# Kernel tuning notes

Measured on AMD Instinct MI355X. Metric: run time of the kernel, lower is better.

The kernel has to match this reference:

```python
import jax, jax.numpy as jnp
import numpy as np

H, HK, D, BLK, GH = 32, 8, 96, 64, 128   # q heads, kv heads, head_dim, gate block, gate hidden
HIDDEN = 3072
THR = 0.03
NEG = -1e30

def _rot_half(x):
    h = x.shape[-1] // 2
    return jnp.concatenate([-x[..., h:], x[..., :h]], axis=-1)

def setup_inputs() -> dict:
    key = jax.random.key(0)
    ks = jax.random.split(key, 6)
    B, S = 1, 2048
    hidden_states = jax.random.normal(ks[0], (B, S, HIDDEN), dtype=jnp.float32)
    # RoPE tables, theta = 10000
    inv_freq = 1.0 / (10000.0 ** (np.arange(0, D, 2, dtype=np.float32) / D))
    t = np.arange(S, dtype=np.float32)
    freqs = np.outer(t, inv_freq)                   # [S, D/2]
    emb = np.concatenate([freqs, freqs], axis=-1)   # [S, D]
    cos = jnp.asarray(np.cos(emb), dtype=jnp.float32)
    sin = jnp.asarray(np.sin(emb), dtype=jnp.float32)
    op = H * D + 2 * HK * D
    qkv_w = jax.random.normal(ks[1], (HIDDEN, op), dtype=jnp.float32) * 0.02
    o_w = jax.random.normal(ks[2], (H * D, HIDDEN), dtype=jnp.float32) * 0.02
    gate_wq = jax.random.normal(ks[3], (D, GH), dtype=jnp.float32) * 0.05
    gate_wk = jax.random.normal(ks[4], (2 * D, GH), dtype=jnp.float32) * 0.05
    return dict(hidden_states=hidden_states, cos=cos, sin=sin,
                qkv_w=qkv_w, o_w=o_w, gate_wq=gate_wq, gate_wk=gate_wk)

def reference(hidden_states, cos, sin, qkv_w, o_w, gate_wq, gate_wk):
    B, S, _ = hidden_states.shape
    G = H // HK            # GQA group size
    nB = S // BLK          # number of gate blocks
    scale = D ** -0.5

    # fused QKV projection and head split
    qkv = hidden_states @ qkv_w
    q = qkv[..., : H * D].reshape(B, S, H, D)
    k = qkv[..., H * D : H * D + HK * D].reshape(B, S, HK, D)
    v = qkv[..., H * D + HK * D :].reshape(B, S, HK, D)
    q_nope, k_nope = q, k

    # RoPE (unsqueeze over head dim)
    cs = cos[None, :, None, :]
    sn = sin[None, :, None, :]
    q = q * cs + _rot_half(q) * sn
    k = k * cs + _rot_half(k) * sn

    # ---- learned block-sparse gate (SeerAttention AttnGate) ----
    kb = k_nope.reshape(B, nB, BLK, HK, D)
    k_pool = jnp.concatenate([kb.mean(2), kb.max(2)], axis=-1)      # [B,nB,HK,2D] avg+max seq pooling
    k_gate = jnp.einsum('bnhe,eg->bnhg', k_pool, gate_wk)
    q_pool = q_nope.reshape(B, S, HK, G, D).mean(3)                 # q-head pooling to kv heads
    q_pool = q_pool.reshape(B, nB, BLK, HK, D).mean(2)              # block pooling
    q_gate = jnp.einsum('bnhd,dg->bnhg', q_pool, gate_wq)
    gate_logits = jnp.einsum('bqhg,bkhg->bhqk', q_gate, k_gate) * (GH ** -0.5)
    blk_causal = jnp.tril(jnp.ones((nB, nB), dtype=bool))
    gate_logits = jnp.where(blk_causal, gate_logits, NEG)
    gate_probs = jax.nn.softmax(gate_logits, axis=-1)
    block_mask = (gate_probs >= THR) & blk_causal                   # threshold sparsity method
    block_mask = block_mask | jnp.eye(nB, dtype=bool)               # diagonal block always active

    # expand block mask to token level, intersect with causal mask
    tok_mask = jnp.repeat(jnp.repeat(block_mask, BLK, axis=2), BLK, axis=3)  # [B,HK,S,S]
    causal = jnp.tril(jnp.ones((S, S), dtype=bool))
    mask = tok_mask & causal

    # ---- block-sparse masked attention with GQA ----
    qh = q.transpose(0, 2, 1, 3).reshape(B, HK, G, S, D)
    kh = k.transpose(0, 2, 1, 3)                                    # [B,HK,S,D]
    vh = v.transpose(0, 2, 1, 3)
    scores = jnp.einsum('bhgsd,bhtd->bhgst', qh, kh) * scale
    scores = jnp.where(mask[:, :, None], scores, NEG)
    attn = jax.nn.softmax(scores, axis=-1)
    out = jnp.einsum('bhgst,bhtd->bhgsd', attn, vh)                 # [B,HK,G,S,D]
    out = out.reshape(B, H, S, D).transpose(0, 2, 1, 3).reshape(B, S, H * D)
    return out @ o_w
```

## Files before the change

kernel.cpp:

```cpp
#include <hip/hip_runtime.h>
#include <hip/hip_bf16.h>
#include <math.h>

#define S_LEN 2048
#define HID 3072
#define NHEAD 32
#define NKV 8
#define HDIM 96
#define QKV_N 4608
#define NB 32
#define GHDIM 128

typedef __attribute__((ext_vector_type(8))) short bf16x8;
typedef __attribute__((ext_vector_type(4))) float f32x4;
typedef unsigned short ushort_t;

__device__ __forceinline__ unsigned short f2bf(float x) {
    unsigned u = __float_as_uint(x);
    u += 0x7fffu + ((u >> 16) & 1u);
    return (unsigned short)(u >> 16);
}
__device__ __forceinline__ unsigned packbf2(float a, float b) {
    return (unsigned)f2bf(a) | ((unsigned)f2bf(b) << 16);
}

#define GLOBAL_AS __attribute__((address_space(1)))
#define LDS_AS __attribute__((address_space(3)))
__device__ __forceinline__ void gl_lds16(const void* g, void* l) {
    __builtin_amdgcn_global_load_lds((const GLOBAL_AS unsigned int*)g,
                                     (LDS_AS unsigned int*)l, 16, 0, 0);
}

__global__ __launch_bounds__(256, 2) void gemm_bf16(const ushort_t* __restrict__ A,
                                                    const ushort_t* __restrict__ Bt,
                                                    float* __restrict__ C,
                                                    int M, int N, int K) {
    __shared__ ushort_t As[128 * 64];
    __shared__ ushort_t Bs[128 * 64];
    const int tid = threadIdx.x;
    const int lane = tid & 63;
    const int w = tid >> 6;
    const int wm = (w >> 1) * 64;
    const int wn = (w & 1) * 64;
    const int l15 = lane & 15;
    const int quad = lane >> 4;
    const int m0 = blockIdx.y * 128;
    const int n0 = blockIdx.x * 128;

    f32x4 acc[4][4] = {};

    for (int k0 = 0; k0 < K; k0 += 64) {
        __syncthreads();
#pragma unroll
        for (int j = 0; j < 4; ++j) {
            int s = j * 256 + w * 64 + lane;
            int row = s >> 3;
            int kc = (s & 7) ^ (row & 7);
            gl_lds16(A + (size_t)(m0 + row) * K + k0 + kc * 8,
                     &As[(j * 256 + w * 64) * 8]);
        }
#pragma unroll
        for (int j = 0; j < 4; ++j) {
            int s = j * 256 + w * 64 + lane;
            int row = s >> 3;
            int kc = (s & 7) ^ (row & 7);
            gl_lds16(Bt + (size_t)(n0 + row) * K + k0 + kc * 8,
                     &Bs[(j * 256 + w * 64) * 8]);
        }
        __syncthreads();
        bf16x8 af[2][4], bf[2][4];
#pragma unroll
        for (int mt = 0; mt < 4; ++mt) {
            int row = wm + mt * 16 + l15;
            int rx = row & 7;
#pragma unroll
            for (int ph = 0; ph < 2; ++ph)
                af[ph][mt] = *(const bf16x8*)&As[(row * 8 + ((ph * 4 + quad) ^ rx)) * 8];
        }
#pragma unroll
        for (int nt = 0; nt < 4; ++nt) {
            int row = wn + nt * 16 + l15;
            int rx = row & 7;
#pragma unroll
            for (int ph = 0; ph < 2; ++ph)
                bf[ph][nt] = *(const bf16x8*)&Bs[(row * 8 + ((ph * 4 + quad) ^ rx)) * 8];
        }
#pragma unroll
        for (int ph = 0; ph < 2; ++ph)
#pragma unroll
            for (int mt = 0; mt < 4; ++mt)
#pragma unroll
                for (int nt = 0; nt < 4; ++nt)
                    acc[mt][nt] = __builtin_amdgcn_mfma_f32_16x16x32_bf16(
                        af[ph][mt], bf[ph][nt], acc[mt][nt], 0, 0, 0);
    }
#pragma unroll
    for (int mt = 0; mt < 4; ++mt)
#pragma unroll
        for (int nt = 0; nt < 4; ++nt)
#pragma unroll
            for (int r = 0; r < 4; ++r) {
                int row = m0 + wm + mt * 16 + quad * 4 + r;
                int col = n0 + wn + nt * 16 + l15;
                C[(size_t)row * N + col] = acc[mt][nt][r];
            }
}

__global__ __launch_bounds__(256) void conv_bf16(const float* __restrict__ X,
                                                 ushort_t* __restrict__ Y, int n4) {
    int i = blockIdx.x * 256 + threadIdx.x;
    if (i >= n4) return;
    const float4 v = *(const float4*)(X + (size_t)i * 4);
    int2 p;
    p.x = (int)packbf2(v.x, v.y);
    p.y = (int)packbf2(v.z, v.w);
    *(int2*)(Y + (size_t)i * 4) = p;
}

__global__ __launch_bounds__(256) void transpose_convert(const float* __restrict__ W,
                                                         ushort_t* __restrict__ Wt,
                                                         int K, int N) {
    __shared__ float Ts[64][65];
    const int k0 = blockIdx.y * 64, n0 = blockIdx.x * 64;
    const int tid = threadIdx.x;
    {
        int r = tid >> 2, cq = tid & 3;
#pragma unroll
        for (int i = 0; i < 4; ++i) {
            int c = cq * 16 + i * 4;
            const float4 v = *(const float4*)(W + (size_t)(k0 + r) * N + n0 + c);
            Ts[r][c] = v.x; Ts[r][c + 1] = v.y; Ts[r][c + 2] = v.z; Ts[r][c + 3] = v.w;
        }
    }
    __syncthreads();
#pragma unroll
    for (int it = 0; it < 2; ++it) {
        int n = (tid >> 3) + it * 32;
        int kc = tid & 7;
        int4 r;
        r.x = (int)(packbf2(Ts[kc * 8 + 0][n], Ts[kc * 8 + 1][n]));
        r.y = (int)(packbf2(Ts[kc * 8 + 2][n], Ts[kc * 8 + 3][n]));
        r.z = (int)(packbf2(Ts[kc * 8 + 4][n], Ts[kc * 8 + 5][n]));
        r.w = (int)(packbf2(Ts[kc * 8 + 6][n], Ts[kc * 8 + 7][n]));
        *(int4*)(Wt + (size_t)(n0 + n) * K + k0 + kc * 8) = r;
    }
}

__global__ __launch_bounds__(128) void pool_gate_k_kernel(const float* __restrict__ qkv,
                                                          const float* __restrict__ gate_wk,
                                                          float* __restrict__ k_gate) {
    int nb = blockIdx.x, h = blockIdx.y;
    int tid = threadIdx.x;
    __shared__ float pool[192];
    if (tid < 96) {
        float s = 0.f, mx = -1e30f;
        for (int i = 0; i < 64; i++) {
            float v = qkv[(size_t)(nb * 64 + i) * QKV_N + HID + h * 96 + tid];
            s += v;
            mx = fmaxf(mx, v);
        }
        pool[tid] = s * (1.f / 64.f);
        pool[96 + tid] = mx;
    }
    __syncthreads();
    float acc = 0.f;
    for (int e = 0; e < 192; e++) acc += pool[e] * gate_wk[e * GHDIM + tid];
    k_gate[(size_t)(nb * NKV + h) * GHDIM + tid] = acc;
}

__global__ __launch_bounds__(128) void pool_gate_q_kernel(const float* __restrict__ qkv,
                                                          const float* __restrict__ gate_wq,
                                                          float* __restrict__ q_gate) {
    int nb = blockIdx.x, h = blockIdx.y;
    int tid = threadIdx.x;
    __shared__ float pool[96];
    if (tid < 96) {
        float s = 0.f;
        for (int i = 0; i < 64; i++)
            for (int g = 0; g < 4; g++)
                s += qkv[(size_t)(nb * 64 + i) * QKV_N + (h * 4 + g) * 96 + tid];
        pool[tid] = s * (1.f / 256.f);
    }
    __syncthreads();
    float acc = 0.f;
    for (int e = 0; e < 96; e++) acc += pool[e] * gate_wq[e * GHDIM + tid];
    q_gate[(size_t)(nb * NKV + h) * GHDIM + tid] = acc;
}

__global__ __launch_bounds__(64) void blockmask_kernel(const float* __restrict__ q_gate,
                                                       const float* __restrict__ k_gate,
                                                       int* __restrict__ mask) {
    int h = blockIdx.x, qb = blockIdx.y;
    int tid = threadIdx.x;
    __shared__ float logits[32];
    if (tid < 32) {
        if (tid <= qb) {
            float acc = 0.f;
            const float* qg = &q_gate[(size_t)(qb * NKV + h) * GHDIM];
            const float* kg = &k_gate[(size_t)(tid * NKV + h) * GHDIM];
            for (int e = 0; e < GHDIM; e++) acc += qg[e] * kg[e];
            logits[tid] = acc * 0.08838834764831845f;
        } else {
            logits[tid] = -1e30f;
        }
    }
    __syncthreads();
    if (tid < 32) {
        float mx = -1e30f;
        for (int j = 0; j <= qb; j++) mx = fmaxf(mx, logits[j]);
        float sum = 0.f;
        for (int j = 0; j <= qb; j++) sum += __expf(logits[j] - mx);
        float p = (tid <= qb) ? __expf(logits[tid] - mx) / sum : 0.f;
        int m = ((p >= 0.03f) && (tid <= qb)) || (tid == qb);
        mask[(h * NB + qb) * NB + tid] = m;
    }
}

__global__ __launch_bounds__(256) void rope_q_kernel(const float* __restrict__ qkv,
                                                     const float* __restrict__ cosb,
                                                     const float* __restrict__ sinb,
                                                     ushort_t* __restrict__ Qb) {
    int idx = blockIdx.x * 256 + threadIdx.x;
    int d = idx % 48;
    int tmp = idx / 48;
    int head = tmp % 32;
    int s = tmp / 32;
    size_t base = (size_t)s * QKV_N + head * 96;
    float x0 = qkv[base + d];
    float x1 = qkv[base + d + 48];
    float c0 = cosb[s * 96 + d], c1 = cosb[s * 96 + d + 48];
    float s0 = sinb[s * 96 + d], s1 = sinb[s * 96 + d + 48];
    size_t ob = (size_t)s * HID + head * 96;
    Qb[ob + d] = f2bf(x0 * c0 - x1 * s0);
    Qb[ob + d + 48] = f2bf(x1 * c1 + x0 * s1);
}

__global__ __launch_bounds__(256) void rope_k_kernel(const float* __restrict__ qkv,
                                                     const float* __restrict__ cosb,
                                                     const float* __restrict__ sinb,
                                                     ushort_t* __restrict__ Kb) {
    int idx = blockIdx.x * 256 + threadIdx.x;
    int d = idx % 48;
    int tmp = idx / 48;
    int h = tmp % 8;
    int s = tmp / 8;
    size_t base = (size_t)s * QKV_N + HID + h * 96;
    float x0 = qkv[base + d];
    float x1 = qkv[base + d + 48];
    float c0 = cosb[s * 96 + d], c1 = cosb[s * 96 + d + 48];
    float s0 = sinb[s * 96 + d], s1 = sinb[s * 96 + d + 48];
    size_t ob = ((size_t)h * S_LEN + s) * 128;
    Kb[ob + d] = f2bf(x0 * c0 - x1 * s0);
    Kb[ob + d + 48] = f2bf(x1 * c1 + x0 * s1);
}

__global__ __launch_bounds__(256) void transpose_v_kernel(const float* __restrict__ qkv,
                                                          ushort_t* __restrict__ Vtb) {
    __shared__ float Vs[64][97];
    const int ibk = blockIdx.x, h = blockIdx.y;
    const int tid = threadIdx.x;
    {
        int t = tid >> 2, cq = tid & 3;
#pragma unroll
        for (int i = 0; i < 6; ++i) {
            int c = cq * 24 + i * 4;
            const float4 v = *(const float4*)(qkv + (size_t)(ibk * 64 + t) * QKV_N +
                                              HID + 768 + h * 96 + c);
            Vs[t][c] = v.x; Vs[t][c + 1] = v.y; Vs[t][c + 2] = v.z; Vs[t][c + 3] = v.w;
        }
    }
    __syncthreads();
#pragma unroll
    for (int it = 0; it < 3; ++it) {
        int s = tid + it * 256;
        int d = s >> 3, tc = s & 7;
        int4 r;
        r.x = (int)(packbf2(Vs[tc * 8 + 0][d], Vs[tc * 8 + 1][d]));
        r.y = (int)(packbf2(Vs[tc * 8 + 2][d], Vs[tc * 8 + 3][d]));
        r.z = (int)(packbf2(Vs[tc * 8 + 4][d], Vs[tc * 8 + 5][d]));
        r.w = (int)(packbf2(Vs[tc * 8 + 6][d], Vs[tc * 8 + 7][d]));
        *(int4*)(Vtb + ((size_t)h * 96 + d) * S_LEN + ibk * 64 + tc * 8) = r;
    }
}

__global__ __launch_bounds__(256) void attn_mfma(const ushort_t* __restrict__ Qb,
                                                 const ushort_t* __restrict__ Kb,
                                                 const ushort_t* __restrict__ Vtb,
                                                 const int* __restrict__ mask,
                                                 ushort_t* __restrict__ out) {
    const int hq = blockIdx.x;
    const int ib = NB - 1 - blockIdx.y;
    const int h = hq >> 2;
    const int tid = threadIdx.x;
    const int lane = tid & 63;
    const int w = tid >> 6;
    const int l15 = lane & 15;
    const int quad = lane >> 4;

    __shared__ ushort_t Ks[64 * 128];
    __shared__ ushort_t Vt[96 * 64];
    __shared__ ushort_t Ps[64][72];

    bf16x8 qf[3];
    {
        const ushort_t* qp = Qb + (size_t)(ib * 64 + w * 16 + l15) * HID + hq * 96;
#pragma unroll
        for (int ks = 0; ks < 3; ++ks)
            qf[ks] = *(const bf16x8*)(qp + ks * 32 + quad * 8);
    }

    float m_i[4], l_i[4];
#pragma unroll
    for (int r = 0; r < 4; ++r) { m_i[r] = -1e30f; l_i[r] = 0.f; }
    f32x4 acc_o[6] = {};
    const float scale = 0.10206207261596575f;

    const ushort_t* kbase = Kb + (size_t)h * S_LEN * 128;
    const ushort_t* vbase = Vtb + (size_t)h * 96 * S_LEN;

    for (int jb = 0; jb <= ib; ++jb) {
        if (!mask[(h * NB + ib) * NB + jb]) continue;
        __syncthreads();
#pragma unroll
        for (int j = 0; j < 4; ++j) {
            int s = j * 256 + w * 64 + lane;
            int t = s >> 4;
            int dc = (s & 15) ^ (t & 7);
            gl_lds16(kbase + (size_t)(jb * 64 + t) * 128 + dc * 8,
                     &Ks[(j * 256 + w * 64) * 8]);
        }
#pragma unroll
        for (int j = 0; j < 3; ++j) {
            int s = j * 256 + w * 64 + lane;
            int d = s >> 3;
            int tc = (s & 7) ^ (d & 7);
            gl_lds16(vbase + (size_t)d * S_LEN + jb * 64 + tc * 8,
                     &Vt[(j * 256 + w * 64) * 8]);
        }
        __syncthreads();

        f32x4 s4[4] = {};
#pragma unroll
        for (int ks = 0; ks < 3; ++ks)
#pragma unroll
            for (int nt = 0; nt < 4; ++nt) {
                int t = nt * 16 + l15;
                int slot = (ks * 4 + quad) ^ (t & 7);
                bf16x8 kb = *(const bf16x8*)&Ks[(t * 16 + slot) * 8];
                s4[nt] = __builtin_amdgcn_mfma_f32_16x16x32_bf16(qf[ks], kb, s4[nt], 0, 0, 0);
            }
#pragma unroll
        for (int nt = 0; nt < 4; ++nt)
#pragma unroll
            for (int r = 0; r < 4; ++r) {
                float v = s4[nt][r] * scale;
                if (jb == ib && (nt * 16 + l15) > (w * 16 + quad * 4 + r)) v = -1e30f;
                s4[nt][r] = v;
            }
        float alpha[4];
#pragma unroll
        for (int r = 0; r < 4; ++r) {
            float mx = fmaxf(fmaxf(s4[0][r], s4[1][r]), fmaxf(s4[2][r], s4[3][r]));
            mx = fmaxf(mx, __shfl_xor(mx, 1));
            mx = fmaxf(mx, __shfl_xor(mx, 2));
            mx = fmaxf(mx, __shfl_xor(mx, 4));
            mx = fmaxf(mx, __shfl_xor(mx, 8));
            float mnew = fmaxf(m_i[r], mx);
            alpha[r] = __expf(m_i[r] - mnew);
            float ps = 0.f;
#pragma unroll
            for (int nt = 0; nt < 4; ++nt) {
                float p = __expf(s4[nt][r] - mnew);
                s4[nt][r] = p;
                ps += p;
            }
            ps += __shfl_xor(ps, 1);
            ps += __shfl_xor(ps, 2);
            ps += __shfl_xor(ps, 4);
            ps += __shfl_xor(ps, 8);
            l_i[r] = l_i[r] * alpha[r] + ps;
            m_i[r] = mnew;
        }
#pragma unroll
        for (int t = 0; t < 6; ++t)
#pragma unroll
            for (int r = 0; r < 4; ++r) acc_o[t][r] *= alpha[r];
#pragma unroll
        for (int nt = 0; nt < 4; ++nt)
#pragma unroll
            for (int r = 0; r < 4; ++r)
                Ps[w * 16 + quad * 4 + r][nt * 16 + l15] = (short)f2bf(s4[nt][r]);
#pragma unroll
        for (int ks = 0; ks < 2; ++ks) {
            bf16x8 pa = *(const bf16x8*)&Ps[w * 16 + l15][ks * 32 + quad * 8];
#pragma unroll
            for (int t = 0; t < 6; ++t) {
                int d = t * 16 + l15;
                int slot = (ks * 4 + quad) ^ (d & 7);
                bf16x8 vb = *(const bf16x8*)&Vt[(d * 8 + slot) * 8];
                acc_o[t] = __builtin_amdgcn_mfma_f32_16x16x32_bf16(pa, vb, acc_o[t], 0, 0, 0);
            }
        }
    }
#pragma unroll
    for (int r = 0; r < 4; ++r) {
        float inv = 1.f / l_i[r];
        int row = ib * 64 + w * 16 + quad * 4 + r;
#pragma unroll
        for (int t = 0; t < 6; ++t)
            out[(size_t)row * HID + hq * 96 + t * 16 + l15] = f2bf(acc_o[t][r] * inv);
    }
}

extern "C" void kernel_launch(void* const* d_in, const int* in_sizes, int n_in,
                              void* d_out, int out_size, void* d_ws, size_t ws_size,
                              hipStream_t stream) {
    const float* hidden  = (const float*)d_in[0];
    const float* cosb    = (const float*)d_in[1];
    const float* sinb    = (const float*)d_in[2];
    const float* qkv_w   = (const float*)d_in[3];
    const float* o_w     = (const float*)d_in[4];
    const float* gate_wq = (const float*)d_in[5];
    const float* gate_wk = (const float*)d_in[6];
    float* out = (float*)d_out;

    char* ws = (char*)d_ws;
    float*    qkv   = (float*)ws;
    ushort_t* h_bf  = (ushort_t*)(ws + 37748736);
    ushort_t* w1t   = (ushort_t*)(ws + 50331648);
    ushort_t* attn_out = (ushort_t*)(ws + 78643200);
    ushort_t* Kb    = (ushort_t*)(ws + 91226112);
    ushort_t* Vtb   = (ushort_t*)(ws + 95420416);
    float* k_gate   = (float*)(ws + 98566144);
    float* q_gate   = (float*)(ws + 98697216);
    int*   mask     = (int*)(ws + 98828288);
    ushort_t* Qb    = h_bf;
    ushort_t* o_wt  = w1t;

    conv_bf16<<<(S_LEN * HID / 4 + 255) / 256, 256, 0, stream>>>(hidden, h_bf, S_LEN * HID / 4);
    transpose_convert<<<dim3(QKV_N / 64, HID / 64), 256, 0, stream>>>(qkv_w, w1t, HID, QKV_N);
    gemm_bf16<<<dim3(QKV_N / 128, S_LEN / 128), 256, 0, stream>>>(h_bf, w1t, qkv, S_LEN, QKV_N, HID);
    pool_gate_k_kernel<<<dim3(NB, NKV), 128, 0, stream>>>(qkv, gate_wk, k_gate);
    pool_gate_q_kernel<<<dim3(NB, NKV), 128, 0, stream>>>(qkv, gate_wq, q_gate);
    blockmask_kernel<<<dim3(NKV, NB), 64, 0, stream>>>(q_gate, k_gate, mask);
    rope_q_kernel<<<S_LEN * 32 * 48 / 256, 256, 0, stream>>>(qkv, cosb, sinb, Qb);
    rope_k_kernel<<<S_LEN * 8 * 48 / 256, 256, 0, stream>>>(qkv, cosb, sinb, Kb);
    transpose_v_kernel<<<dim3(NB, NKV), 256, 0, stream>>>(qkv, Vtb);
    transpose_convert<<<dim3(HID / 64, HID / 64), 256, 0, stream>>>(o_w, o_wt, HID, HID);
    attn_mfma<<<dim3(NHEAD, NB), 256, 0, stream>>>(Qb, Kb, Vtb, mask, attn_out);
    gemm_bf16<<<dim3(HID / 128, S_LEN / 128), 256, 0, stream>>>(attn_out, o_wt, out, S_LEN, HID, HID);
}
```

Baseline: 411.8 us.

## Double-buffer K/V tiles in sparse attention and fuse Q/K RoPE kernels

The attention kernel now builds a ballot bitmask of active key blocks, iterates only those, and double-buffers K and V tiles in LDS so the next block's global-to-LDS load overlaps the current block's MFMA work, using raw barriers and vmcnt waits. K is stored with a 96-wide stride and a rotated-chunk layout instead of 128 padding, which cuts bytes moved. The softmax scale and log2(e) are folded into Q during RoPE so the kernel can use exp2 directly, and the Q and K RoPE kernels are merged into one launch. o_wt is moved to the qkv buffer; the hand-written waitcnt counts and layout math risk subtle races or bank conflicts.

```diff
diff --git a/kernel.cpp b/kernel.cpp
--- a/kernel.cpp
+++ b/kernel.cpp
@@ -15,6 +15,8 @@
 typedef __attribute__((ext_vector_type(4))) float f32x4;
 typedef unsigned short ushort_t;
 
+#define SCALE2 0.14724444754f
+
 __device__ __forceinline__ unsigned short f2bf(float x) {
     unsigned u = __float_as_uint(x);
     u += 0x7fffu + ((u >> 16) & 1u);
@@ -29,6 +31,9 @@
 __device__ __forceinline__ void gl_lds16(const void* g, void* l) {
     __builtin_amdgcn_global_load_lds((const GLOBAL_AS unsigned int*)g,
                                      (LDS_AS unsigned int*)l, 16, 0, 0);
+}
+__device__ __forceinline__ void barrier_raw() {
+    asm volatile("s_barrier" ::: "memory");
 }
 
 __global__ __launch_bounds__(256, 2) void gemm_bf16(const ushort_t* __restrict__ A,
@@ -216,42 +221,32 @@
     }
 }
 
-__global__ __launch_bounds__(256) void rope_q_kernel(const float* __restrict__ qkv,
-                                                     const float* __restrict__ cosb,
-                                                     const float* __restrict__ sinb,
-                                                     ushort_t* __restrict__ Qb) {
+__global__ __launch_bounds__(256) void rope_qk_kernel(const float* __restrict__ qkv,
+                                                      const float* __restrict__ cosb,
+                                                      const float* __restrict__ sinb,
+                                                      ushort_t* __restrict__ Qb,
+                                                      ushort_t* __restrict__ Kb) {
     int idx = blockIdx.x * 256 + threadIdx.x;
     int d = idx % 48;
     int tmp = idx / 48;
-    int head = tmp % 32;
-    int s = tmp / 32;
-    size_t base = (size_t)s * QKV_N + head * 96;
-    float x0 = qkv[base + d];
-    float x1 = qkv[base + d + 48];
+    int head = tmp % 40;
+    int s = tmp / 40;
     float c0 = cosb[s * 96 + d], c1 = cosb[s * 96 + d + 48];
     float s0 = sinb[s * 96 + d], s1 = sinb[s * 96 + d + 48];
-    size_t ob = (size_t)s * HID + head * 96;
-    Qb[ob + d] = f2bf(x0 * c0 - x1 * s0);
-    Qb[ob + d + 48] = f2bf(x1 * c1 + x0 * s1);
-}
-
-__global__ __launch_bounds__(256) void rope_k_kernel(const float* __restrict__ qkv,
-                                                     const float* __restrict__ cosb,
-                                                     const float* __restrict__ sinb,
-                                                     ushort_t* __restrict__ Kb) {
-    int idx = blockIdx.x * 256 + threadIdx.x;
-    int d = idx % 48;
-    int tmp = idx / 48;
-    int h = tmp % 8;
-    int s = tmp / 8;
-    size_t base = (size_t)s * QKV_N + HID + h * 96;
-    float x0 = qkv[base + d];
-    float x1 = qkv[base + d + 48];
-    float c0 = cosb[s * 96 + d], c1 = cosb[s * 96 + d + 48];
-    float s0 = sinb[s * 96 + d], s1 = sinb[s * 96 + d + 48];
-    size_t ob = ((size_t)h * S_LEN + s) * 128;
-    Kb[ob + d] = f2bf(x0 * c0 - x1 * s0);
-    Kb[ob + d + 48] = f2bf(x1 * c1 + x0 * s1);
+    if (head < 32) {
+        size_t base = (size_t)s * QKV_N + head * 96;
+        float x0 = qkv[base + d], x1 = qkv[base + d + 48];
+        size_t ob = (size_t)s * HID + head * 96;
+        Qb[ob + d] = f2bf((x0 * c0 - x1 * s0) * SCALE2);
+        Qb[ob + d + 48] = f2bf((x1 * c1 + x0 * s1) * SCALE2);
+    } else {
+        int hh = head - 32;
+        size_t base = (size_t)s * QKV_N + HID + hh * 96;
+        float x0 = qkv[base + d], x1 = qkv[base + d + 48];
+        size_t ob = ((size_t)hh * S_LEN + s) * 96;
+        Kb[ob + d] = f2bf(x0 * c0 - x1 * s0);
+        Kb[ob + d + 48] = f2bf(x1 * c1 + x0 * s1);
+    }
 }
 
 __global__ __launch_bounds__(256) void transpose_v_kernel(const float* __restrict__ qkv,
@@ -289,7 +284,7 @@
                                                  const int* __restrict__ mask,
                                                  ushort_t* __restrict__ out) {
     const int hq = blockIdx.x;
-    const int ib = NB - 1 - blockIdx.y;
+    const int ib = NB - 1 - (int)blockIdx.y;
     const int h = hq >> 2;
     const int tid = threadIdx.x;
     const int lane = tid & 63;
@@ -297,9 +292,21 @@
     const int l15 = lane & 15;
     const int quad = lane >> 4;
 
-    __shared__ ushort_t Ks[64 * 128];
-    __shared__ ushort_t Vt[96 * 64];
+    __shared__ ushort_t KsL[2][64 * 96];
+    __shared__ ushort_t VtL[2][96 * 64];
     __shared__ ushort_t Ps[64][72];
+
+    int pk[3];
+    {
+        int b0 = quad + (l15 & 7);
+#pragma unroll
+        for (int ks = 0; ks < 3; ++ks) {
+            int p = b0 + ks * 4;
+            if (p >= 12) p -= 12;
+            if (p >= 12) p -= 12;
+            pk[ks] = p;
+        }
+    }
 
     bf16x8 qf[3];
     {
@@ -309,25 +316,27 @@
             qf[ks] = *(const bf16x8*)(qp + ks * 32 + quad * 8);
     }
 
+    const ushort_t* kbase = Kb + (size_t)h * S_LEN * 96;
+    const ushort_t* vbase = Vtb + (size_t)h * 96 * S_LEN;
+
+    unsigned long long bits =
+        __ballot((lane <= ib) && (mask[(h * NB + ib) * NB + (lane & 31)] != 0));
+
     float m_i[4], l_i[4];
 #pragma unroll
     for (int r = 0; r < 4; ++r) { m_i[r] = -1e30f; l_i[r] = 0.f; }
     f32x4 acc_o[6] = {};
-    const float scale = 0.10206207261596575f;
-
-    const ushort_t* kbase = Kb + (size_t)h * S_LEN * 128;
-    const ushort_t* vbase = Vtb + (size_t)h * 96 * S_LEN;
-
-    for (int jb = 0; jb <= ib; ++jb) {
-        if (!mask[(h * NB + ib) * NB + jb]) continue;
-        __syncthreads();
-#pragma unroll
-        for (int j = 0; j < 4; ++j) {
+
+    auto stage = [&](int jb, int buf) {
+#pragma unroll
+        for (int j = 0; j < 3; ++j) {
             int s = j * 256 + w * 64 + lane;
-            int t = s >> 4;
-            int dc = (s & 15) ^ (t & 7);
-            gl_lds16(kbase + (size_t)(jb * 64 + t) * 128 + dc * 8,
-                     &Ks[(j * 256 + w * 64) * 8]);
+            int t = (s * 2731) >> 15;
+            int cpos = s - t * 12;
+            int c = cpos - (t & 7);
+            if (c < 0) c += 12;
+            gl_lds16(kbase + (size_t)(jb * 64 + t) * 96 + c * 8,
+                     &KsL[buf][(j * 256 + w * 64) * 8]);
         }
 #pragma unroll
         for (int j = 0; j < 3; ++j) {
@@ -335,28 +344,47 @@
             int d = s >> 3;
             int tc = (s & 7) ^ (d & 7);
             gl_lds16(vbase + (size_t)d * S_LEN + jb * 64 + tc * 8,
-                     &Vt[(j * 256 + w * 64) * 8]);
-        }
-        __syncthreads();
+                     &VtL[buf][(j * 256 + w * 64) * 8]);
+        }
+    };
+
+    int jb = (int)__builtin_ctzll(bits);
+    bits &= bits - 1;
+    stage(jb, 0);
+    int cur = 0;
+
+    while (true) {
+        int jn = -1;
+        if (bits) {
+            jn = (int)__builtin_ctzll(bits);
+            bits &= bits - 1;
+        }
+        if (jn >= 0) {
+            stage(jn, cur ^ 1);
+            asm volatile("s_waitcnt vmcnt(6)" ::: "memory");
+        } else {
+            asm volatile("s_waitcnt vmcnt(0)" ::: "memory");
+        }
+        barrier_raw();
+
+        const ushort_t* Kc = KsL[cur];
+        const ushort_t* Vc = VtL[cur];
 
         f32x4 s4[4] = {};
 #pragma unroll
         for (int ks = 0; ks < 3; ++ks)
 #pragma unroll
             for (int nt = 0; nt < 4; ++nt) {
-                int t = nt * 16 + l15;
-                int slot = (ks * 4 + quad) ^ (t & 7);
-                bf16x8 kb = *(const bf16x8*)&Ks[(t * 16 + slot) * 8];
+                bf16x8 kb = *(const bf16x8*)&Kc[(nt * 16 + l15) * 96 + pk[ks] * 8];
                 s4[nt] = __builtin_amdgcn_mfma_f32_16x16x32_bf16(qf[ks], kb, s4[nt], 0, 0, 0);
             }
-#pragma unroll
-        for (int nt = 0; nt < 4; ++nt)
-#pragma unroll
-            for (int r = 0; r < 4; ++r) {
-                float v = s4[nt][r] * scale;
-                if (jb == ib && (nt * 16 + l15) > (w * 16 + quad * 4 + r)) v = -1e30f;
-                s4[nt][r] = v;
-            }
+        if (jb == ib) {
+#pragma unroll
+            for (int nt = 0; nt < 4; ++nt)
+#pragma unroll
+                for (int r = 0; r < 4; ++r)
+                    if ((nt * 16 + l15) > (w * 16 + quad * 4 + r)) s4[nt][r] = -1e30f;
+        }
         float alpha[4];
 #pragma unroll
         for (int r = 0; r < 4; ++r) {
@@ -366,11 +394,11 @@
             mx = fmaxf(mx, __shfl_xor(mx, 4));
             mx = fmaxf(mx, __shfl_xor(mx, 8));
             float mnew = fmaxf(m_i[r], mx);
-            alpha[r] = __expf(m_i[r] - mnew);
+            alpha[r] = __builtin_amdgcn_exp2f(m_i[r] - mnew);
             float ps = 0.f;
 #pragma unroll
             for (int nt = 0; nt < 4; ++nt) {
-                float p = __expf(s4[nt][r] - mnew);
+                float p = __builtin_amdgcn_exp2f(s4[nt][r] - mnew);
                 s4[nt][r] = p;
                 ps += p;
             }
@@ -397,11 +425,18 @@
             for (int t = 0; t < 6; ++t) {
                 int d = t * 16 + l15;
                 int slot = (ks * 4 + quad) ^ (d & 7);
-                bf16x8 vb = *(const bf16x8*)&Vt[(d * 8 + slot) * 8];
+                bf16x8 vb = *(const bf16x8*)&Vc[(d * 8 + slot) * 8];
                 acc_o[t] = __builtin_amdgcn_mfma_f32_16x16x32_bf16(pa, vb, acc_o[t], 0, 0, 0);
             }
         }
-    }
+
+        if (jn < 0) break;
+        asm volatile("s_waitcnt lgkmcnt(0)" ::: "memory");
+        barrier_raw();
+        jb = jn;
+        cur ^= 1;
+    }
+
 #pragma unroll
     for (int r = 0; r < 4; ++r) {
         float inv = 1.f / l_i[r];
@@ -435,7 +470,7 @@
     float* q_gate   = (float*)(ws + 98697216);
     int*   mask     = (int*)(ws + 98828288);
     ushort_t* Qb    = h_bf;
-    ushort_t* o_wt  = w1t;
+    ushort_t* o_wt  = (ushort_t*)qkv;
 
     conv_bf16<<<(S_LEN * HID / 4 + 255) / 256, 256, 0, stream>>>(hidden, h_bf, S_LEN * HID / 4);
     transpose_convert<<<dim3(QKV_N / 64, HID / 64), 256, 0, stream>>>(qkv_w, w1t, HID, QKV_N);
@@ -443,8 +478,7 @@
     pool_gate_k_kernel<<<dim3(NB, NKV), 128, 0, stream>>>(qkv, gate_wk, k_gate);
     pool_gate_q_kernel<<<dim3(NB, NKV), 128, 0, stream>>>(qkv, gate_wq, q_gate);
     blockmask_kernel<<<dim3(NKV, NB), 64, 0, stream>>>(q_gate, k_gate, mask);
-    rope_q_kernel<<<S_LEN * 32 * 48 / 256, 256, 0, stream>>>(qkv, cosb, sinb, Qb);
-    rope_k_kernel<<<S_LEN * 8 * 48 / 256, 256, 0, stream>>>(qkv, cosb, sinb, Kb);
+    rope_qk_kernel<<<S_LEN * 40 * 48 / 256, 256, 0, stream>>>(qkv, cosb, sinb, Qb, Kb);
     transpose_v_kernel<<<dim3(NB, NKV), 256, 0, stream>>>(qkv, Vtb);
     transpose_convert<<<dim3(HID / 64, HID / 64), 256, 0, stream>>>(o_w, o_wt, HID, HID);
     attn_mfma<<<dim3(NHEAD, NB), 256, 0, stream>>>(Qb, Kb, Vtb, mask, attn_out);
```

Result: no change. 413.9 us (+0.5%).
